# Kernel optimization log

Measured on AMD Instinct MI355X. Metric: run time of the kernel, lower is better.

The kernel has to match this reference:

```python
import jax, jax.numpy as jnp
import numpy as np

D_IN = 1024
D_OUT = 1024
NUM_HEADS = 16
HEAD_DIM = D_OUT // NUM_HEADS


def setup_inputs() -> dict:
    key = jax.random.key(0)
    ks = jax.random.split(key, 6)
    s = 0.02
    x = jax.random.normal(ks[0], (1, 4096, D_IN), dtype=jnp.float32)
    Wq = jax.random.normal(ks[1], (D_OUT, D_IN), dtype=jnp.float32) * s
    Wk = jax.random.normal(ks[2], (D_OUT, D_IN), dtype=jnp.float32) * s
    Wv = jax.random.normal(ks[3], (D_OUT, D_IN), dtype=jnp.float32) * s
    Wo = jax.random.normal(ks[4], (D_OUT, D_OUT), dtype=jnp.float32) * s
    bo = jax.random.normal(ks[5], (D_OUT,), dtype=jnp.float32) * s
    return {"x": x, "Wq": Wq, "Wk": Wk, "Wv": Wv, "Wo": Wo, "bo": bo}


def reference(x, Wq, Wk, Wv, Wo, bo):
    b, n, _ = x.shape
    # torch Linear: y = x @ W.T  (no qkv bias)
    q = (x @ Wq.T).reshape(b, n, NUM_HEADS, HEAD_DIM).transpose(0, 2, 1, 3)  # [b,h,n,d]
    k = (x @ Wk.T).reshape(b, n, NUM_HEADS, HEAD_DIM).transpose(0, 2, 1, 3)
    v = (x @ Wv.T).reshape(b, n, NUM_HEADS, HEAD_DIM).transpose(0, 2, 1, 3)
    scores = jnp.einsum("bhqd,bhkd->bhqk", q, k)  # full [b,h,n,n] matrix (naive MHA)
    causal = jnp.triu(jnp.ones((n, n), dtype=bool), k=1)
    scores = jnp.where(causal, -jnp.inf, scores)
    weights = jax.nn.softmax(scores / jnp.sqrt(jnp.float32(HEAD_DIM)), axis=-1)
    ctx = jnp.einsum("bhqk,bhkd->bhqd", weights, v)
    ctx = ctx.transpose(0, 2, 1, 3).reshape(b, n, D_OUT)
    return ctx @ Wo.T + bo
```

## Files before the change

kernel.cpp:

```cpp
#include <hip/hip_runtime.h>
#include <cmath>

#define TOKENS 4096
#define DMODEL 1024
#define NHEADS 16
#define HDIM 64

typedef _Float16 f16;
typedef _Float16 half8 __attribute__((ext_vector_type(8)));
typedef float f32x4 __attribute__((ext_vector_type(4)));

__device__ __forceinline__ void* lds_chunk(void* base, int row, int chunk) {
    int p = chunk ^ (row & 7);
    return (char*)base + row * 128 + p * 16;
}

__device__ __forceinline__ void gload16(const void* g, void* lds) {
    __builtin_amdgcn_global_load_lds(
        (const __attribute__((address_space(1))) unsigned int*)g,
        (__attribute__((address_space(3))) unsigned int*)lds, 16, 0, 0);
}

__global__ __launch_bounds__(256)
void cvt_all(const float* __restrict__ x,  const float* __restrict__ Wq,
             const float* __restrict__ Wk, const float* __restrict__ Wv,
             const float* __restrict__ Wo,
             f16* xh, f16* Wqh, f16* Wkh, f16* Wvh, f16* Woh)
{
    int i = blockIdx.x * 256 + threadIdx.x;
    const float* src; f16* dst; int off;
    if      (i < 524288) { src = x;  dst = xh;  off = i; }
    else if (i < 655360) { src = Wq; dst = Wqh; off = i - 524288; }
    else if (i < 786432) { src = Wk; dst = Wkh; off = i - 655360; }
    else if (i < 917504) { src = Wv; dst = Wvh; off = i - 786432; }
    else                 { src = Wo; dst = Woh; off = i - 917504; }
    float4 a = ((const float4*)src)[off * 2];
    float4 b = ((const float4*)src)[off * 2 + 1];
    half8 hv;
    hv[0] = (f16)a.x; hv[1] = (f16)a.y; hv[2] = (f16)a.z; hv[3] = (f16)a.w;
    hv[4] = (f16)b.x; hv[5] = (f16)b.y; hv[6] = (f16)b.z; hv[7] = (f16)b.w;
    ((half8*)dst)[off] = hv;
}

__global__ __launch_bounds__(256)
void transpose_v(const f16* __restrict__ V, f16* __restrict__ Vt)
{
    __shared__ f16 T[64][66];
    const int tid = threadIdx.x;
    const int t0 = blockIdx.x * 64, d0 = blockIdx.y * 64;
    const int r = tid >> 3, c = (tid & 7) * 8;
#pragma unroll
    for (int it = 0; it < 2; ++it) {
        int row = r + it * 32;
        half8 v = *(const half8*)(V + (size_t)(t0 + row) * DMODEL + d0 + c);
#pragma unroll
        for (int j = 0; j < 8; ++j) T[row][c + j] = v[j];
    }
    __syncthreads();
#pragma unroll
    for (int it = 0; it < 2; ++it) {
        int drow = r + it * 32;
        half8 v;
#pragma unroll
        for (int j = 0; j < 8; ++j) v[j] = T[c + j][drow];
        *(half8*)(Vt + (size_t)(d0 + drow) * TOKENS + t0 + c) = v;
    }
}

template<int MODE>
__global__ __launch_bounds__(256)
void gemm_f16(const f16* __restrict__ A, const f16* __restrict__ W0,
              const f16* __restrict__ W1, const f16* __restrict__ W2,
              const float* __restrict__ bias,
              f16* __restrict__ O0, f16* __restrict__ O1, f16* __restrict__ O2,
              float* __restrict__ Of, int K)
{
    __shared__ __align__(16) f16 As[128 * 64];
    __shared__ __align__(16) f16 Bs[128 * 64];
    const int tid = threadIdx.x, lane = tid & 63, wv = tid >> 6;
    const int g = lane >> 4, ln15 = lane & 15;
    const int bm = blockIdx.y, bn = blockIdx.x;
    const int rowInCall = lane >> 3, p = lane & 7;

    const f16* W = W0;
    f16* Oq = O0;
    int ncol0 = bn * 128;
    if (MODE == 0) {
        int which = bn >> 3;
        W  = which == 0 ? W0 : (which == 1 ? W1 : W2);
        Oq = which == 0 ? O0 : (which == 1 ? O1 : O2);
        ncol0 = (bn & 7) * 128;
    }

    f32x4 acc[4][4] = {};
    const size_t rowB = (size_t)K * 2;
    const int wm = (wv >> 1) * 64, wn = (wv & 1) * 64;

    for (int kt = 0; kt < K / 64; ++kt) {
        if (kt) __syncthreads();
        for (int c = wv * 4; c < wv * 4 + 4; ++c) {
            int r = c * 8 + rowInCall;
            int gc = p ^ (r & 7);
            const char* ga = (const char*)A + (size_t)(bm * 128 + r) * rowB + kt * 128 + gc * 16;
            gload16(ga, (char*)As + c * 1024);
            const char* gb = (const char*)W + (size_t)(ncol0 + r) * rowB + kt * 128 + gc * 16;
            gload16(gb, (char*)Bs + c * 1024);
        }
        __syncthreads();

#pragma unroll
        for (int ks = 0; ks < 2; ++ks) {
            half8 a[4], b[4];
#pragma unroll
            for (int mf = 0; mf < 4; ++mf)
                a[mf] = *(const half8*)lds_chunk(As, wm + mf * 16 + ln15, ks * 4 + g);
#pragma unroll
            for (int nf = 0; nf < 4; ++nf)
                b[nf] = *(const half8*)lds_chunk(Bs, wn + nf * 16 + ln15, ks * 4 + g);
#pragma unroll
            for (int mf = 0; mf < 4; ++mf)
#pragma unroll
                for (int nf = 0; nf < 4; ++nf)
                    acc[mf][nf] = __builtin_amdgcn_mfma_f32_16x16x32_f16(
                        a[mf], b[nf], acc[mf][nf], 0, 0, 0);
        }
    }

#pragma unroll
    for (int mf = 0; mf < 4; ++mf)
#pragma unroll
        for (int nf = 0; nf < 4; ++nf)
#pragma unroll
            for (int r = 0; r < 4; ++r) {
                int row = bm * 128 + wm + mf * 16 + g * 4 + r;
                int col = wn + nf * 16 + ln15;
                if (MODE == 0) {
                    Oq[(size_t)row * 1024 + ncol0 + col] = (f16)acc[mf][nf][r];
                } else {
                    int gc2 = bn * 128 + col;
                    Of[(size_t)row * 1024 + gc2] = acc[mf][nf][r] + bias[gc2];
                }
            }
}

__global__ __launch_bounds__(256)
void attn_f16(const f16* __restrict__ Qf, const f16* __restrict__ Kf,
              const f16* __restrict__ Vt, f16* __restrict__ Ctx)
{
    __shared__ __align__(16) f16 Ks[2][64 * 64];
    __shared__ __align__(16) f16 Vs[2][64 * 64];
    __shared__ __align__(16) f16 Ps[4][16 * 64];
    const int tid = threadIdx.x, lane = tid & 63, wv = tid >> 6;
    const int g = lane >> 4, ln15 = lane & 15;
    const int h = blockIdx.y;
    const int rowInCall = lane >> 3, p = lane & 7;
    char* Pb = (char*)Ps[wv];

    half8 b_ones;
#pragma unroll
    for (int j = 0; j < 8; ++j) b_ones[j] = (f16)1.0f;

    for (int ph = 0; ph < 2; ++ph) {
        const int qb = ph ? (63 - blockIdx.x) : blockIdx.x;

        const int qrow = qb * 64 + wv * 16 + ln15;
        half8 qfr[2];
#pragma unroll
        for (int ks = 0; ks < 2; ++ks) {
            qfr[ks] = *(const half8*)(Qf + (size_t)qrow * DMODEL + h * HDIM + ks * 32 + g * 8);
#pragma unroll
            for (int j = 0; j < 8; ++j) qfr[ks][j] = qfr[ks][j] * (f16)0.125f;
        }

        f32x4 O[4] = {};
        f32x4 Osum = {};
        float m_r[4] = {-1e30f, -1e30f, -1e30f, -1e30f};
        const int qrow_g = qb * 64 + wv * 16 + g * 4;

        auto stage = [&](int kb, int bi) {
            for (int c = wv * 2; c < wv * 2 + 2; ++c) {
                int r = c * 8 + rowInCall;
                int gc = p ^ (r & 7);
                const char* gk = (const char*)Kf + (size_t)(kb * 64 + r) * (DMODEL * 2)
                                 + h * 128 + gc * 16;
                gload16(gk, (char*)&Ks[bi][0] + c * 1024);
                const char* gv = (const char*)Vt + (size_t)(h * 64 + r) * (TOKENS * 2)
                                 + kb * 128 + gc * 16;
                gload16(gv, (char*)&Vs[bi][0] + c * 1024);
            }
        };

        stage(0, 0);
        __syncthreads();
        int cur = 0;

        for (int kb = 0; kb <= qb; ++kb) {
            if (kb < qb) stage(kb + 1, cur ^ 1);

            f32x4 s[4] = {};
            __builtin_amdgcn_s_setprio(1);
#pragma unroll
            for (int ks = 0; ks < 2; ++ks)
#pragma unroll
                for (int tf = 0; tf < 4; ++tf) {
                    half8 b = *(const half8*)lds_chunk(&Ks[cur][0], tf * 16 + ln15, ks * 4 + g);
                    s[tf] = __builtin_amdgcn_mfma_f32_16x16x32_f16(qfr[ks], b, s[tf], 0, 0, 0);
                }
            __builtin_amdgcn_s_setprio(0);

            const bool diag = (kb == qb);
            float tmax[4] = {-1e30f, -1e30f, -1e30f, -1e30f};
#pragma unroll
            for (int tf = 0; tf < 4; ++tf) {
                int t = kb * 64 + tf * 16 + ln15;
#pragma unroll
                for (int r = 0; r < 4; ++r) {
                    float v = s[tf][r];
                    if (diag && t > qrow_g + r) v = -1e30f;
                    s[tf][r] = v;
                    tmax[r] = fmaxf(tmax[r], v);
                }
            }
#pragma unroll
            for (int r = 0; r < 4; ++r)
#pragma unroll
                for (int mm = 1; mm < 16; mm <<= 1)
                    tmax[r] = fmaxf(tmax[r], __shfl_xor(tmax[r], mm, 64));

            float corr[4];
#pragma unroll
            for (int r = 0; r < 4; ++r) {
                float mnew = fmaxf(m_r[r], tmax[r]);
                corr[r] = __expf(m_r[r] - mnew);
                m_r[r] = mnew;
            }

#pragma unroll
            for (int tf = 0; tf < 4; ++tf)
#pragma unroll
                for (int r = 0; r < 4; ++r) {
                    float e = __expf(s[tf][r] - m_r[r]);
                    int row = g * 4 + r;
                    int t = tf * 16 + ln15;
                    int pc = (t >> 3) ^ (row & 7);
                    *(f16*)(Pb + row * 128 + pc * 16 + (t & 7) * 2) = (f16)e;
                }

#pragma unroll
            for (int df = 0; df < 4; ++df)
#pragma unroll
                for (int r = 0; r < 4; ++r)
                    O[df][r] *= corr[r];
#pragma unroll
            for (int r = 0; r < 4; ++r) Osum[r] *= corr[r];

            asm volatile("s_waitcnt lgkmcnt(0)" ::: "memory");
            __builtin_amdgcn_sched_barrier(0);

            __builtin_amdgcn_s_setprio(1);
#pragma unroll
            for (int ks = 0; ks < 2; ++ks) {
                half8 pa = *(const half8*)lds_chunk(Pb, ln15, ks * 4 + g);
                Osum = __builtin_amdgcn_mfma_f32_16x16x32_f16(pa, b_ones, Osum, 0, 0, 0);
#pragma unroll
                for (int df = 0; df < 4; ++df) {
                    half8 b = *(const half8*)lds_chunk(&Vs[cur][0], df * 16 + ln15, ks * 4 + g);
                    O[df] = __builtin_amdgcn_mfma_f32_16x16x32_f16(pa, b, O[df], 0, 0, 0);
                }
            }
            __builtin_amdgcn_s_setprio(0);

            __syncthreads();
            cur ^= 1;
        }

#pragma unroll
        for (int df = 0; df < 4; ++df)
#pragma unroll
            for (int r = 0; r < 4; ++r) {
                int row = qrow_g + r;
                int col = h * HDIM + df * 16 + ln15;
                Ctx[(size_t)row * DMODEL + col] = (f16)(O[df][r] / Osum[r]);
            }
    }
}

extern "C" void kernel_launch(void* const* d_in, const int* in_sizes, int n_in,
                              void* d_out, int out_size, void* d_ws, size_t ws_size,
                              hipStream_t stream)
{
    const float* x  = (const float*)d_in[0];
    const float* Wq = (const float*)d_in[1];
    const float* Wk = (const float*)d_in[2];
    const float* Wv = (const float*)d_in[3];
    const float* Wo = (const float*)d_in[4];
    const float* bo = (const float*)d_in[5];
    float* out = (float*)d_out;

    const size_t XN = (size_t)TOKENS * DMODEL;
    const size_t WN = (size_t)DMODEL * DMODEL;
    f16* xh  = (f16*)d_ws;
    f16* Wqh = xh  + XN;
    f16* Wkh = Wqh + WN;
    f16* Wvh = Wkh + WN;
    f16* Woh = Wvh + WN;
    f16* Q   = Woh + WN;
    f16* Kb  = Q   + XN;
    f16* Vb  = Kb  + XN;
    f16* Vtb = Vb  + XN;
    f16* Ctx = Vtb + XN;

    cvt_all<<<4096, 256, 0, stream>>>(x, Wq, Wk, Wv, Wo, xh, Wqh, Wkh, Wvh, Woh);

    gemm_f16<0><<<dim3(24, 32), 256, 0, stream>>>(xh, Wqh, Wkh, Wvh, nullptr,
                                                  Q, Kb, Vb, nullptr, DMODEL);
    transpose_v<<<dim3(TOKENS / 64, DMODEL / 64), 256, 0, stream>>>(Vb, Vtb);
    attn_f16<<<dim3(32, NHEADS), 256, 0, stream>>>(Q, Kb, Vtb, Ctx);
    gemm_f16<1><<<dim3(8, 32), 256, 0, stream>>>(Ctx, Woh, nullptr, nullptr, bo,
                                                 nullptr, nullptr, nullptr, out, DMODEL);
}
```

Measured before the change: 246.8 us.

## Fold softmax scale into Q projection, transpose score MFMA, lazy rescale, XCD-aware grid

The Q projection epilogue now multiplies by 0.125*log2(e), so attention can use exp2 directly and no longer scales Q in the kernel. The score MFMA swaps its operands so each lane holds one query column, which removes the 16-lane max reductions and lets P be written with packed 64-bit stores. Rescaling of the output accumulators is skipped unless the max grows by more than 8 (a lazy-rescale threshold). The attention grid is flattened to 1024 single-tile blocks with an XCD-aware mapping of heads and query blocks, replacing the paired-tile loop of 512 blocks. The trade-off is more blocks with uneven work per block, plus a small precision risk from the lazy rescale and round-toward-zero conversion.

```diff
diff --git a/kernel.cpp b/kernel.cpp
--- a/kernel.cpp
+++ b/kernel.cpp
@@ -8,7 +8,11 @@
 
 typedef _Float16 f16;
 typedef _Float16 half8 __attribute__((ext_vector_type(8)));
+typedef __fp16 fp16x2 __attribute__((ext_vector_type(2)));
 typedef float f32x4 __attribute__((ext_vector_type(4)));
+
+#define EXP2F(x) __builtin_amdgcn_exp2f(x)
+#define SCALE_Q 0.18033688011112042f
 
 __device__ __forceinline__ void* lds_chunk(void* base, int row, int chunk) {
     int p = chunk ^ (row & 7);
@@ -85,8 +89,9 @@
     const f16* W = W0;
     f16* Oq = O0;
     int ncol0 = bn * 128;
+    int which = 0;
     if (MODE == 0) {
-        int which = bn >> 3;
+        which = bn >> 3;
         W  = which == 0 ? W0 : (which == 1 ? W1 : W2);
         Oq = which == 0 ? O0 : (which == 1 ? O1 : O2);
         ncol0 = (bn & 7) * 128;
@@ -134,11 +139,13 @@
             for (int r = 0; r < 4; ++r) {
                 int row = bm * 128 + wm + mf * 16 + g * 4 + r;
                 int col = wn + nf * 16 + ln15;
+                float val = acc[mf][nf][r];
                 if (MODE == 0) {
-                    Oq[(size_t)row * 1024 + ncol0 + col] = (f16)acc[mf][nf][r];
+                    if (which == 0) val *= SCALE_Q;
+                    Oq[(size_t)row * 1024 + ncol0 + col] = (f16)val;
                 } else {
                     int gc2 = bn * 128 + col;
-                    Of[(size_t)row * 1024 + gc2] = acc[mf][nf][r] + bias[gc2];
+                    Of[(size_t)row * 1024 + gc2] = val + bias[gc2];
                 }
             }
 }
@@ -152,137 +159,135 @@
     __shared__ __align__(16) f16 Ps[4][16 * 64];
     const int tid = threadIdx.x, lane = tid & 63, wv = tid >> 6;
     const int g = lane >> 4, ln15 = lane & 15;
-    const int h = blockIdx.y;
     const int rowInCall = lane >> 3, p = lane & 7;
+
+    const int id = blockIdx.x;
+    const int xcd = id & 7, slot = id >> 3;
+    const int c_ = slot & 31, j_ = slot >> 5;
+    const int h  = xcd * 2 + (j_ >> 1);
+    const int qb = (j_ & 1) ? (63 - c_) : c_;
+
     char* Pb = (char*)Ps[wv];
 
     half8 b_ones;
 #pragma unroll
     for (int j = 0; j < 8; ++j) b_ones[j] = (f16)1.0f;
 
-    for (int ph = 0; ph < 2; ++ph) {
-        const int qb = ph ? (63 - blockIdx.x) : blockIdx.x;
-
-        const int qrow = qb * 64 + wv * 16 + ln15;
-        half8 qfr[2];
+    const int qrow = qb * 64 + wv * 16 + ln15;
+    half8 qfr[2];
+#pragma unroll
+    for (int ks = 0; ks < 2; ++ks)
+        qfr[ks] = *(const half8*)(Qf + (size_t)qrow * DMODEL + h * HDIM + ks * 32 + g * 8);
+
+    f32x4 O[4] = {};
+    f32x4 Osum = {};
+    float m_q = -1e30f;
+    const int qrow_g = qb * 64 + wv * 16 + g * 4;
+
+    auto stage = [&](int kb, int bi) {
+        for (int c = wv * 2; c < wv * 2 + 2; ++c) {
+            int r = c * 8 + rowInCall;
+            int gc = p ^ (r & 7);
+            const char* gk = (const char*)Kf + (size_t)(kb * 64 + r) * (DMODEL * 2)
+                             + h * 128 + gc * 16;
+            gload16(gk, (char*)&Ks[bi][0] + c * 1024);
+            const char* gv = (const char*)Vt + (size_t)(h * 64 + r) * (TOKENS * 2)
+                             + kb * 128 + gc * 16;
+            gload16(gv, (char*)&Vs[bi][0] + c * 1024);
+        }
+    };
+
+    stage(0, 0);
+    __syncthreads();
+    int cur = 0;
+
+    for (int kb = 0; kb <= qb; ++kb) {
+        if (kb < qb) stage(kb + 1, cur ^ 1);
+
+        f32x4 s[4] = {};
+        __builtin_amdgcn_s_setprio(1);
+#pragma unroll
+        for (int ks = 0; ks < 2; ++ks)
+#pragma unroll
+            for (int tf = 0; tf < 4; ++tf) {
+                half8 a = *(const half8*)lds_chunk(&Ks[cur][0], tf * 16 + ln15, ks * 4 + g);
+                s[tf] = __builtin_amdgcn_mfma_f32_16x16x32_f16(a, qfr[ks], s[tf], 0, 0, 0);
+            }
+        __builtin_amdgcn_s_setprio(0);
+
+        if (kb == qb) {
+#pragma unroll
+            for (int tf = 0; tf < 4; ++tf)
+#pragma unroll
+                for (int r = 0; r < 4; ++r)
+                    if (kb * 64 + tf * 16 + g * 4 + r > qrow) s[tf][r] = -1e30f;
+        }
+
+        float tmax = s[0][0];
+#pragma unroll
+        for (int tf = 0; tf < 4; ++tf)
+#pragma unroll
+            for (int r = 0; r < 4; ++r) tmax = fmaxf(tmax, s[tf][r]);
+        tmax = fmaxf(tmax, __shfl_xor(tmax, 16, 64));
+        tmax = fmaxf(tmax, __shfl_xor(tmax, 32, 64));
+
+        if (!__all(tmax <= m_q + 8.0f)) {
+            float mnew = fmaxf(m_q, tmax);
+            float corr = EXP2F(m_q - mnew);
+            m_q = mnew;
+            float cr[4];
+#pragma unroll
+            for (int r = 0; r < 4; ++r) cr[r] = __shfl(corr, g * 4 + r, 64);
+#pragma unroll
+            for (int df = 0; df < 4; ++df)
+#pragma unroll
+                for (int r = 0; r < 4; ++r) O[df][r] *= cr[r];
+#pragma unroll
+            for (int r = 0; r < 4; ++r) Osum[r] *= cr[r];
+        }
+
+#pragma unroll
+        for (int tf = 0; tf < 4; ++tf) {
+            float e0 = EXP2F(s[tf][0] - m_q);
+            float e1 = EXP2F(s[tf][1] - m_q);
+            float e2 = EXP2F(s[tf][2] - m_q);
+            float e3 = EXP2F(s[tf][3] - m_q);
+            fp16x2 lo = __builtin_amdgcn_cvt_pkrtz(e0, e1);
+            fp16x2 hi = __builtin_amdgcn_cvt_pkrtz(e2, e3);
+            int pc = ((tf << 1) | (g >> 1)) ^ (ln15 & 7);
+            union { fp16x2 h2[2]; double d; } u;
+            u.h2[0] = lo; u.h2[1] = hi;
+            *(double*)(Pb + ln15 * 128 + pc * 16 + (g & 1) * 8) = u.d;
+        }
+
+        asm volatile("s_waitcnt lgkmcnt(0)" ::: "memory");
+        __builtin_amdgcn_sched_barrier(0);
+
+        __builtin_amdgcn_s_setprio(1);
 #pragma unroll
         for (int ks = 0; ks < 2; ++ks) {
-            qfr[ks] = *(const half8*)(Qf + (size_t)qrow * DMODEL + h * HDIM + ks * 32 + g * 8);
-#pragma unroll
-            for (int j = 0; j < 8; ++j) qfr[ks][j] = qfr[ks][j] * (f16)0.125f;
-        }
-
-        f32x4 O[4] = {};
-        f32x4 Osum = {};
-        float m_r[4] = {-1e30f, -1e30f, -1e30f, -1e30f};
-        const int qrow_g = qb * 64 + wv * 16 + g * 4;
-
-        auto stage = [&](int kb, int bi) {
-            for (int c = wv * 2; c < wv * 2 + 2; ++c) {
-                int r = c * 8 + rowInCall;
-                int gc = p ^ (r & 7);
-                const char* gk = (const char*)Kf + (size_t)(kb * 64 + r) * (DMODEL * 2)
-                                 + h * 128 + gc * 16;
-                gload16(gk, (char*)&Ks[bi][0] + c * 1024);
-                const char* gv = (const char*)Vt + (size_t)(h * 64 + r) * (TOKENS * 2)
-                                 + kb * 128 + gc * 16;
-                gload16(gv, (char*)&Vs[bi][0] + c * 1024);
+            half8 pa = *(const half8*)lds_chunk(Pb, ln15, ks * 4 + g);
+            Osum = __builtin_amdgcn_mfma_f32_16x16x32_f16(pa, b_ones, Osum, 0, 0, 0);
+#pragma unroll
+            for (int df = 0; df < 4; ++df) {
+                half8 b = *(const half8*)lds_chunk(&Vs[cur][0], df * 16 + ln15, ks * 4 + g);
+                O[df] = __builtin_amdgcn_mfma_f32_16x16x32_f16(pa, b, O[df], 0, 0, 0);
             }
-        };
-
-        stage(0, 0);
+        }
+        __builtin_amdgcn_s_setprio(0);
+
         __syncthreads();
-        int cur = 0;
-
-        for (int kb = 0; kb <= qb; ++kb) {
-            if (kb < qb) stage(kb + 1, cur ^ 1);
-
-            f32x4 s[4] = {};
-            __builtin_amdgcn_s_setprio(1);
-#pragma unroll
-            for (int ks = 0; ks < 2; ++ks)
-#pragma unroll
-                for (int tf = 0; tf < 4; ++tf) {
-                    half8 b = *(const half8*)lds_chunk(&Ks[cur][0], tf * 16 + ln15, ks * 4 + g);
-                    s[tf] = __builtin_amdgcn_mfma_f32_16x16x32_f16(qfr[ks], b, s[tf], 0, 0, 0);
-                }
-            __builtin_amdgcn_s_setprio(0);
-
-            const bool diag = (kb == qb);
-            float tmax[4] = {-1e30f, -1e30f, -1e30f, -1e30f};
-#pragma unroll
-            for (int tf = 0; tf < 4; ++tf) {
-                int t = kb * 64 + tf * 16 + ln15;
-#pragma unroll
-                for (int r = 0; r < 4; ++r) {
-                    float v = s[tf][r];
-                    if (diag && t > qrow_g + r) v = -1e30f;
-                    s[tf][r] = v;
-                    tmax[r] = fmaxf(tmax[r], v);
-                }
-            }
-#pragma unroll
-            for (int r = 0; r < 4; ++r)
-#pragma unroll
-                for (int mm = 1; mm < 16; mm <<= 1)
-                    tmax[r] = fmaxf(tmax[r], __shfl_xor(tmax[r], mm, 64));
-
-            float corr[4];
-#pragma unroll
-            for (int r = 0; r < 4; ++r) {
-                float mnew = fmaxf(m_r[r], tmax[r]);
-                corr[r] = __expf(m_r[r] - mnew);
-                m_r[r] = mnew;
-            }
-
-#pragma unroll
-            for (int tf = 0; tf < 4; ++tf)
-#pragma unroll
-                for (int r = 0; r < 4; ++r) {
-                    float e = __expf(s[tf][r] - m_r[r]);
-                    int row = g * 4 + r;
-                    int t = tf * 16 + ln15;
-                    int pc = (t >> 3) ^ (row & 7);
-                    *(f16*)(Pb + row * 128 + pc * 16 + (t & 7) * 2) = (f16)e;
-                }
-
-#pragma unroll
-            for (int df = 0; df < 4; ++df)
-#pragma unroll
-                for (int r = 0; r < 4; ++r)
-                    O[df][r] *= corr[r];
-#pragma unroll
-            for (int r = 0; r < 4; ++r) Osum[r] *= corr[r];
-
-            asm volatile("s_waitcnt lgkmcnt(0)" ::: "memory");
-            __builtin_amdgcn_sched_barrier(0);
-
-            __builtin_amdgcn_s_setprio(1);
-#pragma unroll
-            for (int ks = 0; ks < 2; ++ks) {
-                half8 pa = *(const half8*)lds_chunk(Pb, ln15, ks * 4 + g);
-                Osum = __builtin_amdgcn_mfma_f32_16x16x32_f16(pa, b_ones, Osum, 0, 0, 0);
-#pragma unroll
-                for (int df = 0; df < 4; ++df) {
-                    half8 b = *(const half8*)lds_chunk(&Vs[cur][0], df * 16 + ln15, ks * 4 + g);
-                    O[df] = __builtin_amdgcn_mfma_f32_16x16x32_f16(pa, b, O[df], 0, 0, 0);
-                }
-            }
-            __builtin_amdgcn_s_setprio(0);
-
-            __syncthreads();
-            cur ^= 1;
-        }
-
-#pragma unroll
-        for (int df = 0; df < 4; ++df)
-#pragma unroll
-            for (int r = 0; r < 4; ++r) {
-                int row = qrow_g + r;
-                int col = h * HDIM + df * 16 + ln15;
-                Ctx[(size_t)row * DMODEL + col] = (f16)(O[df][r] / Osum[r]);
-            }
-    }
+        cur ^= 1;
+    }
+
+#pragma unroll
+    for (int df = 0; df < 4; ++df)
+#pragma unroll
+        for (int r = 0; r < 4; ++r) {
+            int row = qrow_g + r;
+            int col = h * HDIM + df * 16 + ln15;
+            Ctx[(size_t)row * DMODEL + col] = (f16)(O[df][r] / Osum[r]);
+        }
 }
 
 extern "C" void kernel_launch(void* const* d_in, const int* in_sizes, int n_in,
@@ -315,7 +320,7 @@
     gemm_f16<0><<<dim3(24, 32), 256, 0, stream>>>(xh, Wqh, Wkh, Wvh, nullptr,
                                                   Q, Kb, Vb, nullptr, DMODEL);
     transpose_v<<<dim3(TOKENS / 64, DMODEL / 64), 256, 0, stream>>>(Vb, Vtb);
-    attn_f16<<<dim3(32, NHEADS), 256, 0, stream>>>(Q, Kb, Vtb, Ctx);
+    attn_f16<<<1024, 256, 0, stream>>>(Q, Kb, Vtb, Ctx);
     gemm_f16<1><<<dim3(8, 32), 256, 0, stream>>>(Ctx, Woh, nullptr, nullptr, bo,
                                                  nullptr, nullptr, nullptr, out, DMODEL);
 }
```

Result: faster. 226.8 us (-8.1%).
